# Optimization experiments

Measured on AMD Instinct MI355X. Metric: run time of the kernel, lower is better.

## Reference

```python
import jax, jax.numpy as jnp
import numpy as np

N_NODES = 100000


def setup_inputs() -> dict:
    key = jax.random.key(0)
    ks = jax.random.split(key, 9)
    x = jax.random.normal(ks[0], (N_NODES, 500), dtype=jnp.float32)
    # lin1: Linear(m=500, hidden=64, bias=False) -> weight [hidden, m]
    W1 = jax.random.normal(ks[1], (64, 500), dtype=jnp.float32) * 0.02
    # lin_final: Linear(3*hidden=192, m_y=10, bias=False) -> weight [m_y, 3*hidden]
    Wf = jax.random.normal(ks[2], (10, 192), dtype=jnp.float32) * 0.02
    # 1-hop normalized adjacency in COO form (600k nnz)
    src1 = jax.random.randint(ks[3], (600000,), 0, N_NODES, dtype=jnp.int32)
    dst1 = jax.random.randint(ks[4], (600000,), 0, N_NODES, dtype=jnp.int32)
    val1 = jax.random.uniform(ks[5], (600000,), dtype=jnp.float32)
    # 2-hop normalized adjacency in COO form (1.2M nnz)
    src2 = jax.random.randint(ks[6], (1200000,), 0, N_NODES, dtype=jnp.int32)
    dst2 = jax.random.randint(ks[7], (1200000,), 0, N_NODES, dtype=jnp.int32)
    val2 = jax.random.uniform(ks[8], (1200000,), dtype=jnp.float32)
    return {"x": x, "W1": W1, "Wf": Wf,
            "src1": src1, "dst1": dst1, "val1": val1,
            "src2": src2, "dst2": dst2, "val2": val2}


def _spmm(src, dst, val, h):
    # sparse.mm(A, h): out[dst] += val * h[src]
    return jax.ops.segment_sum(val[:, None] * h[src], dst, num_segments=N_NODES)


def reference(x, W1, Wf, src1, dst1, val1, src2, dst2, val2):
    h = jax.nn.relu(x @ W1.T)                 # [N, hidden]
    h1 = _spmm(src1, dst1, val1, h)           # [N, hidden]
    h2 = _spmm(src2, dst2, val2, h)           # [N, hidden]
    h_final = jnp.concatenate([h, h1, h2], axis=1)  # [N, 3*hidden]
    # dropout is identity in eval mode
    return h_final @ Wf.T                     # [N, m_y]
```

## Files before the change

### kernel.cpp

```cpp
#include <hip/hip_runtime.h>
#include <hip/hip_bf16.h>

#define NN    100000
#define KD    500
#define KP    512
#define HID   64
#define LWS   264
#define GSP   16
#define DB    128
#define NB    782
#define CHUNK 4096

typedef short frag8 __attribute__((ext_vector_type(8)));
typedef float f32x4 __attribute__((ext_vector_type(4)));

static __device__ __forceinline__ unsigned short f2b(float f) {
    return __builtin_bit_cast(unsigned short, __float2bfloat16(f));
}

__global__ __launch_bounds__(256) void k0_w1bf(const float* __restrict__ W1,
                                               unsigned short* __restrict__ W1bf)
{
    const int i = blockIdx.x * 256 + threadIdx.x;
    const int c = i >> 9;
    const int k = i & 511;
    const float v = (k < KD) ? W1[c * KD + k] : 0.f;
    W1bf[i] = f2b(v);
}

__global__ __launch_bounds__(256, 4) void k1_mfma(const float* __restrict__ x,
                                                  const unsigned short* __restrict__ W1bf,
                                                  float* __restrict__ h, int n)
{
    __shared__ unsigned short lw[64 * LWS];
    const int tid   = threadIdx.x;
    const int lane  = tid & 63;
    const int wid   = tid >> 6;
    const int l15   = lane & 15;
    const int l4    = lane >> 4;
    const int koffl = 8 * l4;

    const long rowBlk = (long)blockIdx.x * 64;
    long ra = rowBlk + wid * 16 + l15;
    if (ra >= n) ra = n - 1;
    const float* xp = x + ra * KD + koffl;

    f32x4 acc[4] = {};
    const float4 z = make_float4(0.f, 0.f, 0.f, 0.f);

    for (int c = 0; c < 2; ++c) {
        if (c) __syncthreads();
        #pragma unroll
        for (int it = 0; it < 8; ++it) {
            const int idx = tid + it * 256;
            const int r   = idx >> 5;
            const int q   = idx & 31;
            *(uint4*)&lw[r * LWS + q * 8] =
                *(const uint4*)&W1bf[r * KP + c * 256 + q * 8];
        }
        __syncthreads();

        int k0 = c * 256;
        float4 lo = (k0 + koffl     < KD) ? *(const float4*)(xp + k0)     : z;
        float4 hi = (k0 + koffl + 4 < KD) ? *(const float4*)(xp + k0 + 4) : z;

        #pragma unroll
        for (int ks = 0; ks < 8; ++ks) {
            float4 nlo = z, nhi = z;
            if (ks < 7) {
                const int kn = c * 256 + (ks + 1) * 32;
                nlo = (kn + koffl     < KD) ? *(const float4*)(xp + kn)     : z;
                nhi = (kn + koffl + 4 < KD) ? *(const float4*)(xp + kn + 4) : z;
            }
            frag8 a;
            a[0]=f2b(lo.x); a[1]=f2b(lo.y); a[2]=f2b(lo.z); a[3]=f2b(lo.w);
            a[4]=f2b(hi.x); a[5]=f2b(hi.y); a[6]=f2b(hi.z); a[7]=f2b(hi.w);
            const int koffw = ks * 32 + koffl;
            #pragma unroll
            for (int g = 0; g < 4; ++g) {
                const frag8 b = *(const frag8*)&lw[(g * 16 + l15) * LWS + koffw];
                acc[g] = __builtin_amdgcn_mfma_f32_16x16x32_bf16(a, b, acc[g], 0, 0, 0);
            }
            lo = nlo; hi = nhi;
        }
    }

    #pragma unroll
    for (int r = 0; r < 4; ++r) {
        const long row = rowBlk + wid * 16 + l4 * 4 + r;
        if (row < n) {
            #pragma unroll
            for (int g = 0; g < 4; ++g)
                h[row * HID + g * 16 + l15] = fmaxf(acc[g][r], 0.f);
        }
    }
}

__global__ __launch_bounds__(256) void k2_proj(const float* __restrict__ h,
                                               const float* __restrict__ Wf,
                                               float* __restrict__ out,
                                               float* __restrict__ g1,
                                               float* __restrict__ g2, int n)
{
    __shared__ float lwf[10 * 196];
    const int tid = threadIdx.x;
    for (int idx = tid; idx < 480; idx += 256) {
        const int j = idx / 48;
        const int q = idx - j * 48;
        const float4 v = *(const float4*)&Wf[j * 192 + 4 * q];
        *(float4*)&lwf[j * 196 + 4 * q] = v;
    }
    __syncthreads();

    const long row = (long)blockIdx.x * 8 + (tid >> 5);
    const int  j   = tid & 31;
    if (row < n && j < 30) {
        const int wrow = (j < 10) ? j : ((j < 20) ? j - 10 : j - 20);
        const int coff = (j < 10) ? 0 : ((j < 20) ? 64 : 128);
        const float* wp = &lwf[wrow * 196 + coff];
        const float* hp = &h[row * HID];
        float s = 0.f;
        #pragma unroll
        for (int q = 0; q < 16; ++q) {
            const float4 hv = *(const float4*)&hp[4 * q];
            const float4 wv = *(const float4*)&wp[4 * q];
            s += hv.x * wv.x + hv.y * wv.y + hv.z * wv.z + hv.w * wv.w;
        }
        if (j < 10)      out[row * 10 + j] = s;
        else if (j < 20) g1[row * GSP + (j - 10)] = s;
        else             g2[row * GSP + (j - 20)] = s;
    }
}

__global__ __launch_bounds__(256) void kA_hist(const int* __restrict__ dst1, int nnz1,
                                               const int* __restrict__ dst2, int ntE,
                                               int nblk, int* __restrict__ Cmat)
{
    __shared__ int cnt[NB];
    const int tid = threadIdx.x, blk = blockIdx.x;
    for (int i = tid; i < NB; i += 256) cnt[i] = 0;
    __syncthreads();
    const int base = blk * CHUNK;
    #pragma unroll
    for (int it = 0; it < CHUNK / 256; ++it) {
        const int id = base + it * 256 + tid;
        if (id < ntE) {
            const int d = (id < nnz1) ? dst1[id] : dst2[id - nnz1];
            atomicAdd(&cnt[d / DB], 1);
        }
    }
    __syncthreads();
    for (int b = tid; b < NB; b += 256) Cmat[b * nblk + blk] = cnt[b];
}

__global__ __launch_bounds__(256) void kS1_rowscan(const int* __restrict__ Cmat, int nblk,
                                                   int* __restrict__ OFFmat,
                                                   int* __restrict__ rowSum)
{
    __shared__ int ls[256];
    const int b = blockIdx.x, tid = threadIdx.x;
    const int i0 = 2 * tid, i1 = 2 * tid + 1;
    const int e0 = (i0 < nblk) ? Cmat[b * nblk + i0] : 0;
    const int e1 = (i1 < nblk) ? Cmat[b * nblk + i1] : 0;
    const int ps = e0 + e1;
    ls[tid] = ps;
    __syncthreads();
    for (int off = 1; off < 256; off <<= 1) {
        const int v = (tid >= off) ? ls[tid - off] : 0;
        __syncthreads();
        ls[tid] += v;
        __syncthreads();
    }
    const int excl = ls[tid] - ps;
    if (i0 < nblk) OFFmat[b * nblk + i0] = excl;
    if (i1 < nblk) OFFmat[b * nblk + i1] = excl + e0;
    if (tid == 255) rowSum[b] = ls[255];
}

__global__ __launch_bounds__(256) void kS2_basescan(const int* __restrict__ rowSum,
                                                    int* __restrict__ rowBase)
{
    __shared__ int ls[256];
    const int tid = threadIdx.x;
    int e[4]; int s = 0;
    #pragma unroll
    for (int u = 0; u < 4; ++u) {
        const int i = 4 * tid + u;
        e[u] = (i < NB) ? rowSum[i] : 0;
        s += e[u];
    }
    ls[tid] = s;
    __syncthreads();
    for (int off = 1; off < 256; off <<= 1) {
        const int v = (tid >= off) ? ls[tid - off] : 0;
        __syncthreads();
        ls[tid] += v;
        __syncthreads();
    }
    int run = ls[tid] - s;
    #pragma unroll
    for (int u = 0; u < 4; ++u) {
        const int i = 4 * tid + u;
        if (i < NB) rowBase[i] = run;
        run += e[u];
    }
}

__global__ __launch_bounds__(256) void kC_fill(const int* __restrict__ src1,
                                               const int* __restrict__ dst1,
                                               const float* __restrict__ val1, int nnz1,
                                               const int* __restrict__ src2,
                                               const int* __restrict__ dst2,
                                               const float* __restrict__ val2, int ntE,
                                               int nblk,
                                               const int* __restrict__ OFFmat,
                                               const int* __restrict__ rowBase,
                                               uint2* __restrict__ bins)
{
    __shared__ int cur[NB];
    const int tid = threadIdx.x, blk = blockIdx.x;
    for (int b = tid; b < NB; b += 256)
        cur[b] = rowBase[b] + OFFmat[b * nblk + blk];
    __syncthreads();
    const int base = blk * CHUNK;
    #pragma unroll
    for (int it = 0; it < CHUNK / 256; ++it) {
        const int id = base + it * 256 + tid;
        if (id < ntE) {
            const bool h1 = id < nnz1;
            const int  ii = h1 ? id : id - nnz1;
            const int   s = h1 ? src1[ii] : src2[ii];
            const int   d = h1 ? dst1[ii] : dst2[ii];
            const float v = h1 ? val1[ii] : val2[ii];
            const int   b = d / DB;
            const int slot = atomicAdd(&cur[b], 1);
            uint2 r;
            r.x = (unsigned)s | ((unsigned)(!h1) << 17) | ((unsigned)(d - b * DB) << 18);
            r.y = __builtin_bit_cast(unsigned, v);
            bins[slot] = r;
        }
    }
}

__global__ __launch_bounds__(256) void kD_acc(const uint2* __restrict__ bins,
                                              const int* __restrict__ rowBase,
                                              const int* __restrict__ rowSum,
                                              const float* __restrict__ g1,
                                              const float* __restrict__ g2,
                                              float* __restrict__ out)
{
    __shared__ float lacc[DB * 10];
    const int tid = threadIdx.x, b = blockIdx.x;
    for (int i = tid; i < DB * 10; i += 256) lacc[i] = 0.f;
    __syncthreads();
    const int start = rowBase[b];
    const int cnt   = rowSum[b];
    const int nt    = cnt * 10;
    for (int i = tid; i < nt; i += 256) {
        const int e = (int)((unsigned)i / 10u);
        const int j = i - 10 * e;
        const uint2 r = bins[start + e];
        const int   src = r.x & 0x1FFFF;
        const int   hop = (r.x >> 17) & 1;
        const int   dl  = (int)(r.x >> 18);
        const float v   = __builtin_bit_cast(float, r.y);
        const float* gp = hop ? g2 : g1;
        atomicAdd(&lacc[dl * 10 + j], v * gp[(size_t)src * GSP + j]);
    }
    __syncthreads();
    const int rows = min(DB, NN - b * DB);
    float* op = out + (size_t)b * DB * 10;
    for (int i = tid; i < rows * 10; i += 256)
        op[i] += lacc[i];
}

__global__ __launch_bounds__(256) void k_scatter_dir(const int* __restrict__ src1,
                                                     const int* __restrict__ dst1,
                                                     const float* __restrict__ val1, int n1,
                                                     const int* __restrict__ src2,
                                                     const int* __restrict__ dst2,
                                                     const float* __restrict__ val2, int nt,
                                                     const float* __restrict__ g1,
                                                     const float* __restrict__ g2,
                                                     float* __restrict__ out)
{
    const int t = blockIdx.x * 256 + threadIdx.x;
    if (t >= nt) return;
    const bool h1 = t < n1;
    const int  tt = h1 ? t : t - n1;
    const int  e  = (int)((unsigned)tt / 10u);
    const int  j  = tt - 10 * e;
    const int* sp = h1 ? src1 : src2;
    const int* dp = h1 ? dst1 : dst2;
    const float* vp = h1 ? val1 : val2;
    const float* gp = h1 ? g1 : g2;
    unsafeAtomicAdd(&out[(size_t)dp[e] * 10 + j],
                    vp[e] * gp[(size_t)sp[e] * GSP + j]);
}

extern "C" void kernel_launch(void* const* d_in, const int* in_sizes, int n_in,
                              void* d_out, int out_size, void* d_ws, size_t ws_size,
                              hipStream_t stream)
{
    const float* x    = (const float*)d_in[0];
    const float* W1   = (const float*)d_in[1];
    const float* Wf   = (const float*)d_in[2];
    const int*   src1 = (const int*)d_in[3];
    const int*   dst1 = (const int*)d_in[4];
    const float* val1 = (const float*)d_in[5];
    const int*   src2 = (const int*)d_in[6];
    const int*   dst2 = (const int*)d_in[7];
    const float* val2 = (const float*)d_in[8];
    const int nnz1 = in_sizes[3];
    const int nnz2 = in_sizes[6];
    const int ntE  = nnz1 + nnz2;
    const int n = NN;
    const int nblk = (ntE + CHUNK - 1) / CHUNK;

    char* p = (char*)d_ws;
    unsigned short* W1bf = (unsigned short*)p;       p += (size_t)64 * KP * 2;
    float* h    = (float*)p;                         p += (size_t)NN * HID * 4;
    float* g1   = (float*)p;                         p += (size_t)NN * GSP * 4;
    float* g2   = (float*)p;                         p += (size_t)NN * GSP * 4;
    uint2* bins = (uint2*)p;                         p += (size_t)ntE * 8;
    int* Cmat   = (int*)p;                           p += (size_t)NB * nblk * 4;
    int* OFFmat = (int*)p;                           p += (size_t)NB * nblk * 4;
    int* rowSum = (int*)p;                           p += (size_t)NB * 4;
    int* rowBase= (int*)p;                           p += (size_t)NB * 4;
    float* out  = (float*)d_out;
    const size_t ws_need = (size_t)(p - (char*)d_ws);

    k0_w1bf<<<128, 256, 0, stream>>>(W1, W1bf);
    k1_mfma<<<(n + 63) / 64, 256, 0, stream>>>(x, W1bf, h, n);
    k2_proj<<<(n + 7) / 8, 256, 0, stream>>>(h, Wf, out, g1, g2, n);

    if (ws_size >= ws_need) {
        kA_hist<<<nblk, 256, 0, stream>>>(dst1, nnz1, dst2, ntE, nblk, Cmat);
        kS1_rowscan<<<NB, 256, 0, stream>>>(Cmat, nblk, OFFmat, rowSum);
        kS2_basescan<<<1, 256, 0, stream>>>(rowSum, rowBase);
        kC_fill<<<nblk, 256, 0, stream>>>(src1, dst1, val1, nnz1,
                                          src2, dst2, val2, ntE,
                                          nblk, OFFmat, rowBase, bins);
        kD_acc<<<NB, 256, 0, stream>>>(bins, rowBase, rowSum, g1, g2, out);
    } else {
        const int n1 = 10 * nnz1;
        const int nt = n1 + 10 * nnz2;
        k_scatter_dir<<<(nt + 255) / 256, 256, 0, stream>>>(src1, dst1, val1, n1,
                                                            src2, dst2, val2, nt,
                                                            g1, g2, out);
    }
}
```

Baseline: 265.5 us.

## Shrink destination bins to 32 rows, transpose count matrix, batch LDS atomics

Reduces the destination bin size from 128 to 32 rows, so the accumulation kernel launches about four times as many blocks, each holding fewer edges. The per-chunk count and offset matrices are transposed to block-major order so that the histogram and fill kernels write and read them contiguously. The accumulation loop now issues four independent gathers before doing its shared-memory atomics, to overlap load latency. In exchange, the count and offset matrices and the per-block shared counter arrays are four times larger, and the single-block base scan handles 13 elements per thread.

Result: slower. 274.6 us (+3.4%).

```diff
diff --git a/kernel.cpp b/kernel.cpp
--- a/kernel.cpp
+++ b/kernel.cpp
@@ -7,8 +7,8 @@
 #define HID   64
 #define LWS   264
 #define GSP   16
-#define DB    128
-#define NB    782
+#define DB    32
+#define NB    3125
 #define CHUNK 4096
 
 typedef short frag8 __attribute__((ext_vector_type(8)));
@@ -134,7 +134,7 @@
 
 __global__ __launch_bounds__(256) void kA_hist(const int* __restrict__ dst1, int nnz1,
                                                const int* __restrict__ dst2, int ntE,
-                                               int nblk, int* __restrict__ Cmat)
+                                               int* __restrict__ Cmat)
 {
     __shared__ int cnt[NB];
     const int tid = threadIdx.x, blk = blockIdx.x;
@@ -150,7 +150,7 @@
         }
     }
     __syncthreads();
-    for (int b = tid; b < NB; b += 256) Cmat[b * nblk + blk] = cnt[b];
+    for (int b = tid; b < NB; b += 256) Cmat[(size_t)blk * NB + b] = cnt[b];
 }
 
 __global__ __launch_bounds__(256) void kS1_rowscan(const int* __restrict__ Cmat, int nblk,
@@ -160,8 +160,8 @@
     __shared__ int ls[256];
     const int b = blockIdx.x, tid = threadIdx.x;
     const int i0 = 2 * tid, i1 = 2 * tid + 1;
-    const int e0 = (i0 < nblk) ? Cmat[b * nblk + i0] : 0;
-    const int e1 = (i1 < nblk) ? Cmat[b * nblk + i1] : 0;
+    const int e0 = (i0 < nblk) ? Cmat[(size_t)i0 * NB + b] : 0;
+    const int e1 = (i1 < nblk) ? Cmat[(size_t)i1 * NB + b] : 0;
     const int ps = e0 + e1;
     ls[tid] = ps;
     __syncthreads();
@@ -172,8 +172,8 @@
         __syncthreads();
     }
     const int excl = ls[tid] - ps;
-    if (i0 < nblk) OFFmat[b * nblk + i0] = excl;
-    if (i1 < nblk) OFFmat[b * nblk + i1] = excl + e0;
+    if (i0 < nblk) OFFmat[(size_t)i0 * NB + b] = excl;
+    if (i1 < nblk) OFFmat[(size_t)i1 * NB + b] = excl + e0;
     if (tid == 255) rowSum[b] = ls[255];
 }
 
@@ -182,10 +182,11 @@
 {
     __shared__ int ls[256];
     const int tid = threadIdx.x;
-    int e[4]; int s = 0;
-    #pragma unroll
-    for (int u = 0; u < 4; ++u) {
-        const int i = 4 * tid + u;
+    const int EPT = (NB + 255) / 256;
+    int e[13]; int s = 0;
+    #pragma unroll
+    for (int u = 0; u < 13; ++u) {
+        const int i = tid * EPT + u;
         e[u] = (i < NB) ? rowSum[i] : 0;
         s += e[u];
     }
@@ -199,8 +200,8 @@
     }
     int run = ls[tid] - s;
     #pragma unroll
-    for (int u = 0; u < 4; ++u) {
-        const int i = 4 * tid + u;
+    for (int u = 0; u < 13; ++u) {
+        const int i = tid * EPT + u;
         if (i < NB) rowBase[i] = run;
         run += e[u];
     }
@@ -212,7 +213,6 @@
                                                const int* __restrict__ src2,
                                                const int* __restrict__ dst2,
                                                const float* __restrict__ val2, int ntE,
-                                               int nblk,
                                                const int* __restrict__ OFFmat,
                                                const int* __restrict__ rowBase,
                                                uint2* __restrict__ bins)
@@ -220,7 +220,7 @@
     __shared__ int cur[NB];
     const int tid = threadIdx.x, blk = blockIdx.x;
     for (int b = tid; b < NB; b += 256)
-        cur[b] = rowBase[b] + OFFmat[b * nblk + blk];
+        cur[b] = rowBase[b] + OFFmat[(size_t)blk * NB + b];
     __syncthreads();
     const int base = blk * CHUNK;
     #pragma unroll
@@ -254,23 +254,31 @@
     for (int i = tid; i < DB * 10; i += 256) lacc[i] = 0.f;
     __syncthreads();
     const int start = rowBase[b];
-    const int cnt   = rowSum[b];
-    const int nt    = cnt * 10;
-    for (int i = tid; i < nt; i += 256) {
-        const int e = (int)((unsigned)i / 10u);
-        const int j = i - 10 * e;
-        const uint2 r = bins[start + e];
-        const int   src = r.x & 0x1FFFF;
-        const int   hop = (r.x >> 17) & 1;
-        const int   dl  = (int)(r.x >> 18);
-        const float v   = __builtin_bit_cast(float, r.y);
-        const float* gp = hop ? g2 : g1;
-        atomicAdd(&lacc[dl * 10 + j], v * gp[(size_t)src * GSP + j]);
-    }
-    __syncthreads();
-    const int rows = min(DB, NN - b * DB);
+    const int nt    = rowSum[b] * 10;
+    for (int i0 = tid; i0 < nt; i0 += 1024) {
+        float c[4]; int li[4];
+        #pragma unroll
+        for (int u = 0; u < 4; ++u) {
+            const int i = i0 + u * 256;
+            li[u] = -1;
+            c[u] = 0.f;
+            if (i < nt) {
+                const int e = (int)((unsigned)i / 10u);
+                const int j = i - 10 * e;
+                const uint2 r = bins[start + e];
+                const int   src = r.x & 0x1FFFF;
+                const float* gp = ((r.x >> 17) & 1) ? g2 : g1;
+                c[u]  = __builtin_bit_cast(float, r.y) * gp[(size_t)src * GSP + j];
+                li[u] = (int)(r.x >> 18) * 10 + j;
+            }
+        }
+        #pragma unroll
+        for (int u = 0; u < 4; ++u)
+            if (li[u] >= 0) atomicAdd(&lacc[li[u]], c[u]);
+    }
+    __syncthreads();
     float* op = out + (size_t)b * DB * 10;
-    for (int i = tid; i < rows * 10; i += 256)
+    for (int i = tid; i < DB * 10; i += 256)
         op[i] += lacc[i];
 }
 
@@ -335,12 +343,12 @@
     k2_proj<<<(n + 7) / 8, 256, 0, stream>>>(h, Wf, out, g1, g2, n);
 
     if (ws_size >= ws_need) {
-        kA_hist<<<nblk, 256, 0, stream>>>(dst1, nnz1, dst2, ntE, nblk, Cmat);
+        kA_hist<<<nblk, 256, 0, stream>>>(dst1, nnz1, dst2, ntE, Cmat);
         kS1_rowscan<<<NB, 256, 0, stream>>>(Cmat, nblk, OFFmat, rowSum);
         kS2_basescan<<<1, 256, 0, stream>>>(rowSum, rowBase);
         kC_fill<<<nblk, 256, 0, stream>>>(src1, dst1, val1, nnz1,
                                           src2, dst2, val2, ntE,
-                                          nblk, OFFmat, rowBase, bins);
+                                          OFFmat, rowBase, bins);
         kD_acc<<<NB, 256, 0, stream>>>(bins, rowBase, rowSum, g1, g2, out);
     } else {
         const int n1 = 10 * nnz1;
```
